# Performance work log

Measured on AMD Instinct MI355X. Metric: run time of the kernel, lower is better.

## Reference

```python
import jax, jax.numpy as jnp
import numpy as np


def setup_inputs() -> dict:
    key = jax.random.key(0)
    k1, k2, k3 = jax.random.split(key, 3)
    B, N, D = 4096, 8192, 1024
    protein_features = jax.random.normal(k1, (B, D), dtype=jnp.float32)
    function_features = jax.random.normal(k2, (N, D), dtype=jnp.float32)
    positive_mask = jax.random.randint(k3, (B, N), 0, 2, dtype=jnp.int32)
    temperature = jnp.zeros((1,), dtype=jnp.float32)  # exp(0) = 1
    return {
        "protein_features": protein_features,
        "function_features": function_features,
        "positive_mask": positive_mask,
        "temperature": temperature,
    }


def reference(protein_features, function_features, positive_mask, temperature):
    # logits: [B, N]
    logits = jnp.matmul(protein_features, function_features.T) / jnp.exp(temperature[0])
    # row-wise logsumexp, computed ONCE per row (the torch loop recomputes it per positive)
    lse = jax.nn.logsumexp(logits, axis=1, keepdims=True)  # [B, 1]
    m = (positive_mask == 1).astype(logits.dtype)          # [B, N]
    n_pos = m.sum()
    # per-pair loss = -pos_logit + logsumexp(row); mean over all positive pairs
    loss_sum = ((lse - logits) * m).sum()
    return jnp.where(n_pos > 0, loss_sum / n_pos, jnp.zeros((), dtype=logits.dtype))
```

## Files before the change

kernel.cpp:

```cpp
#include <hip/hip_runtime.h>
#include <hip/hip_bf16.h>

typedef __attribute__((ext_vector_type(4))) float f32x4;
typedef __attribute__((ext_vector_type(8))) __bf16 bf16x8;
typedef __attribute__((ext_vector_type(8))) unsigned short u16x8;

constexpr int BROWS = 4096;
constexpr int NCOLS = 8192;
constexpr int DK    = 1024;
constexpr int BM = 256, BN = 256, BK = 64;
constexpr int NCB = NCOLS / BN;
constexpr int NKT = DK / BK;
constexpr int NIT = NKT / 2;

__device__ static inline unsigned short f2bf(float f) {
  unsigned int u = __builtin_bit_cast(unsigned int, f);
  u += 0x7FFFu + ((u >> 16) & 1u);
  return (unsigned short)(u >> 16);
}

__device__ static inline void gload16(const void* g, void* l) {
  __builtin_amdgcn_global_load_lds(
      (const __attribute__((address_space(1))) void*)g,
      (__attribute__((address_space(3))) void*)l, 16, 0, 0);
}

__global__ void convert_kernel(const float* __restrict__ src,
                               unsigned short* __restrict__ dst,
                               int n4, int applyScale,
                               const float* __restrict__ temp) {
  float scale = applyScale ? expf(-temp[0]) : 1.0f;
  int i = blockIdx.x * blockDim.x + threadIdx.x;
  if (i >= n4) return;
  float4 v = reinterpret_cast<const float4*>(src)[i];
  ushort4 o;
  o.x = f2bf(v.x * scale);
  o.y = f2bf(v.y * scale);
  o.z = f2bf(v.z * scale);
  o.w = f2bf(v.w * scale);
  reinterpret_cast<ushort4*>(dst)[i] = o;
}

__device__ __forceinline__ void stage_half(const unsigned short* __restrict__ g,
                                           unsigned short* l, int t, int kt) {
#pragma unroll
  for (int p = 0; p < 2; ++p) {
    const int off = p * 8192 + t * 16;
    const int row = off >> 7;
    const int keSw = ((off & 127) >> 1) ^ ((row & 7) << 3);
    gload16(g + (size_t)row * DK + kt * 64 + keSw, l + (off >> 1));
  }
}

#define MFMA_BF16 __builtin_amdgcn_mfma_f32_16x16x32_bf16

#define LDS_FRAG(base, row, kk)                                             \
  __builtin_bit_cast(bf16x8, *reinterpret_cast<const u16x8*>(               \
      &(base)[((row) * 64 + (kk) * 32 + l4 * 8) ^ (((row) & 7) << 3)]))

#define READ_A(b, q)                                              \
  aFr[0][0] = LDS_FRAG(As[b][wm], (2*(q)    )*16 + l15, 0);       \
  aFr[0][1] = LDS_FRAG(As[b][wm], (2*(q)    )*16 + l15, 1);       \
  aFr[1][0] = LDS_FRAG(As[b][wm], (2*(q) + 1)*16 + l15, 0);       \
  aFr[1][1] = LDS_FRAG(As[b][wm], (2*(q) + 1)*16 + l15, 1);

#define READ_B(b)                                                 \
  bFr[0][0] = LDS_FRAG(Bs[b][bhB], brB +  0 + l15, 0);            \
  bFr[0][1] = LDS_FRAG(Bs[b][bhB], brB +  0 + l15, 1);            \
  bFr[1][0] = LDS_FRAG(Bs[b][bhB], brB + 16 + l15, 0);            \
  bFr[1][1] = LDS_FRAG(Bs[b][bhB], brB + 16 + l15, 1);            \
  bFr[2][0] = LDS_FRAG(Bs[b][bhB], brB + 32 + l15, 0);            \
  bFr[2][1] = LDS_FRAG(Bs[b][bhB], brB + 32 + l15, 1);            \
  bFr[3][0] = LDS_FRAG(Bs[b][bhB], brB + 48 + l15, 0);            \
  bFr[3][1] = LDS_FRAG(Bs[b][bhB], brB + 48 + l15, 1);

#define COMPUTE(q)                                                                  \
  __builtin_amdgcn_s_setprio(1);                                                   \
  _Pragma("unroll") for (int mm = 0; mm < 2; ++mm)                                  \
  _Pragma("unroll") for (int n = 0; n < 4; ++n) {                                   \
    acc[2*(q)+mm][n] = MFMA_BF16(aFr[mm][0], bFr[n][0], acc[2*(q)+mm][n], 0, 0, 0); \
    acc[2*(q)+mm][n] = MFMA_BF16(aFr[mm][1], bFr[n][1], acc[2*(q)+mm][n], 0, 0, 0); \
  }                                                                                 \
  __builtin_amdgcn_s_setprio(0);

#define PHASE_BAR                          \
  asm volatile("" ::: "memory");           \
  __builtin_amdgcn_s_barrier();            \
  asm volatile("" ::: "memory");

__global__ __launch_bounds__(512, 2)
void main_kernel(const unsigned short* __restrict__ Pb,
                 const unsigned short* __restrict__ Fb,
                 const int* __restrict__ mask,
                 f32x4* __restrict__ partials) {
  __shared__ __align__(16) unsigned short As[2][2][128 * 64];
  __shared__ __align__(16) unsigned short Bs[2][2][128 * 64];
  __shared__ float redM[4][256], redS[4][256], redP[4][256], redC[4][256];

  const int t    = threadIdx.x;
  const int lane = t & 63;
  const int w    = t >> 6;
  const int wm   = w >> 2;
  const int wn   = w & 3;
  const int l15  = lane & 15;
  const int l4   = lane >> 4;
  const int bhB  = wn >> 1;
  const int brB  = (wn & 1) * 64;

  const int brow = blockIdx.y * BM;
  const int bcol = blockIdx.x * BN;

  const unsigned short* Ag0 = Pb + (size_t)brow * DK;
  const unsigned short* Ag1 = Pb + (size_t)(brow + 128) * DK;
  const unsigned short* Bg0 = Fb + (size_t)bcol * DK;
  const unsigned short* Bg1 = Fb + (size_t)(bcol + 128) * DK;

  f32x4 acc[8][4] = {};
  bf16x8 bFr[4][2];
  bf16x8 aFr[2][2];

  stage_half(Bg0, Bs[0][0], t, 0);
  stage_half(Bg1, Bs[0][1], t, 0);
  stage_half(Ag0, As[0][0], t, 0);
  stage_half(Ag1, As[0][1], t, 0);
  stage_half(Bg0, Bs[1][0], t, 1);
  stage_half(Bg1, Bs[1][1], t, 1);
  asm volatile("s_waitcnt vmcnt(4)" ::: "memory");
  PHASE_BAR;

  for (int i = 0; i < NIT; ++i) {
    const int t1 = 2 * i + 1;
    const bool more = (i < NIT - 1);
    READ_B(0); READ_A(0, 0);
    stage_half(Ag0, As[1][0], t, t1);
    COMPUTE(0); PHASE_BAR;
    READ_A(0, 1);
    stage_half(Ag1, As[1][1], t, t1);
    COMPUTE(1); PHASE_BAR;
    READ_A(0, 2);
    if (more) stage_half(Bg0, Bs[0][0], t, t1 + 1);
    COMPUTE(2); PHASE_BAR;
    READ_A(0, 3);
    if (more) stage_half(Bg1, Bs[0][1], t, t1 + 1);
    COMPUTE(3);
    if (more) { asm volatile("s_waitcnt vmcnt(4)" ::: "memory"); }
    else      { asm volatile("s_waitcnt vmcnt(0)" ::: "memory"); }
    PHASE_BAR;
    READ_B(1); READ_A(1, 0);
    if (more) stage_half(Ag0, As[0][0], t, t1 + 1);
    COMPUTE(0); PHASE_BAR;
    READ_A(1, 1);
    if (more) stage_half(Ag1, As[0][1], t, t1 + 1);
    COMPUTE(1); PHASE_BAR;
    READ_A(1, 2);
    if (more) stage_half(Bg0, Bs[1][0], t, t1 + 2);
    COMPUTE(2); PHASE_BAR;
    READ_A(1, 3);
    if (more) stage_half(Bg1, Bs[1][1], t, t1 + 2);
    COMPUTE(3);
    if (more) { asm volatile("s_waitcnt vmcnt(4)" ::: "memory"); }
    PHASE_BAR;
  }

#pragma unroll
  for (int m = 0; m < 8; ++m) {
#pragma unroll
    for (int r = 0; r < 4; ++r) {
      float v0 = acc[m][0][r], v1 = acc[m][1][r], v2 = acc[m][2][r], v3 = acc[m][3][r];
      float mx = fmaxf(fmaxf(v0, v1), fmaxf(v2, v3));
#pragma unroll
      for (int s = 1; s < 16; s <<= 1) mx = fmaxf(mx, __shfl_xor(mx, s, 64));
      float se = __expf(v0 - mx) + __expf(v1 - mx) + __expf(v2 - mx) + __expf(v3 - mx);

      const int lr = wm * 128 + m * 16 + l4 * 4 + r;
      const int* mrow = mask + (size_t)(brow + lr) * NCOLS + bcol + wn * 64 + l15;
      float ps = 0.f, pc = 0.f;
      if (mrow[0]  == 1) { ps += v0; pc += 1.f; }
      if (mrow[16] == 1) { ps += v1; pc += 1.f; }
      if (mrow[32] == 1) { ps += v2; pc += 1.f; }
      if (mrow[48] == 1) { ps += v3; pc += 1.f; }
#pragma unroll
      for (int s = 1; s < 16; s <<= 1) {
        se += __shfl_xor(se, s, 64);
        ps += __shfl_xor(ps, s, 64);
        pc += __shfl_xor(pc, s, 64);
      }
      if (l15 == 0) {
        redM[wn][lr] = mx;
        redS[wn][lr] = se;
        redP[wn][lr] = ps;
        redC[wn][lr] = pc;
      }
    }
  }
  __syncthreads();

  if (t < 256) {
    float m0 = redM[0][t], m1 = redM[1][t], m2 = redM[2][t], m3 = redM[3][t];
    float m  = fmaxf(fmaxf(m0, m1), fmaxf(m2, m3));
    float s  = redS[0][t] * __expf(m0 - m) + redS[1][t] * __expf(m1 - m)
             + redS[2][t] * __expf(m2 - m) + redS[3][t] * __expf(m3 - m);
    float ps = redP[0][t] + redP[1][t] + redP[2][t] + redP[3][t];
    float pc = redC[0][t] + redC[1][t] + redC[2][t] + redC[3][t];
    f32x4 out4;
    out4.x = m; out4.y = s; out4.z = ps; out4.w = pc;
    partials[(size_t)(brow + t) * NCB + blockIdx.x] = out4;
  }
}

__global__ void row_reduce_kernel(const f32x4* __restrict__ partials,
                                  float* __restrict__ rowContrib,
                                  float* __restrict__ rowCnt) {
  const int row  = blockIdx.x * 4 + (threadIdx.x >> 6);
  const int lane = threadIdx.x & 63;
  f32x4 p = partials[(size_t)row * NCB + (lane & 31)];
  float m = p.x;
#pragma unroll
  for (int s = 1; s < 32; s <<= 1) m = fmaxf(m, __shfl_xor(m, s, 64));
  float se = p.y * __expf(p.x - m);
  float ps = p.z, pc = p.w;
#pragma unroll
  for (int s = 1; s < 32; s <<= 1) {
    se += __shfl_xor(se, s, 64);
    ps += __shfl_xor(ps, s, 64);
    pc += __shfl_xor(pc, s, 64);
  }
  if (lane == 0) {
    float lse = m + logf(se);
    rowContrib[row] = pc * lse - ps;
    rowCnt[row]     = pc;
  }
}

__global__ void final_kernel(const float* __restrict__ rowContrib,
                             const float* __restrict__ rowCnt,
                             float* __restrict__ out) {
  __shared__ double sC[256];
  __shared__ double sN[256];
  double c = 0.0, n = 0.0;
  for (int i = threadIdx.x; i < BROWS; i += 256) {
    c += (double)rowContrib[i];
    n += (double)rowCnt[i];
  }
  sC[threadIdx.x] = c;
  sN[threadIdx.x] = n;
  __syncthreads();
  for (int s = 128; s > 0; s >>= 1) {
    if ((int)threadIdx.x < s) {
      sC[threadIdx.x] += sC[threadIdx.x + s];
      sN[threadIdx.x] += sN[threadIdx.x + s];
    }
    __syncthreads();
  }
  if (threadIdx.x == 0) out[0] = (sN[0] > 0.0) ? (float)(sC[0] / sN[0]) : 0.0f;
}

extern "C" void kernel_launch(void* const* d_in, const int* in_sizes, int n_in,
                              void* d_out, int out_size, void* d_ws, size_t ws_size,
                              hipStream_t stream) {
  const float* P    = (const float*)d_in[0];
  const float* F    = (const float*)d_in[1];
  const int*   mask = (const int*)d_in[2];
  const float* temp = (const float*)d_in[3];
  float* out = (float*)d_out;

  char* ws = (char*)d_ws;
  unsigned short* Pb = (unsigned short*)ws;
  unsigned short* Fb = (unsigned short*)(ws + (size_t)BROWS * DK * 2);
  f32x4* partials    = (f32x4*)(ws + (size_t)(BROWS + NCOLS) * DK * 2);
  float* rowContrib  = (float*)((char*)partials + (size_t)BROWS * NCB * sizeof(f32x4));
  float* rowCnt      = rowContrib + BROWS;

  const int nP4 = BROWS * DK / 4;
  const int nF4 = NCOLS * DK / 4;
  hipLaunchKernelGGL(convert_kernel, dim3(nP4 / 256), dim3(256), 0, stream, P, Pb, nP4, 1, temp);
  hipLaunchKernelGGL(convert_kernel, dim3(nF4 / 256), dim3(256), 0, stream, F, Fb, nF4, 0, temp);
  hipLaunchKernelGGL(main_kernel, dim3(NCOLS / BN, BROWS / BM), dim3(512), 0, stream, Pb, Fb, mask, partials);
  hipLaunchKernelGGL(row_reduce_kernel, dim3(BROWS / 4), dim3(256), 0, stream, partials, rowContrib, rowCnt);
  hipLaunchKernelGGL(final_kernel, dim3(1), dim3(256), 0, stream, rowContrib, rowCnt, out);
}
```

Before: 115.3 us.

## Stage mask tiles into LDS asynchronously and pipeline epilogue processing

The positive-mask tile for each 256x256 block is now loaded with async global-to-LDS copies in 32-row chunks, reusing the A/B operand buffers. The first chunk is issued during the last K iteration and the rest are double-buffered against epilogue processing. Previously the epilogue read the mask with scattered direct global loads after the GEMM. This hides mask-load latency behind compute, at the cost of extra barriers, vmcnt bookkeeping and tighter coupling to the staging schedule.

```diff
diff --git a/kernel.cpp b/kernel.cpp
--- a/kernel.cpp
+++ b/kernel.cpp
@@ -52,6 +52,23 @@
   }
 }
 
+__device__ __forceinline__ void stage_mask(const int* __restrict__ mask,
+                                           unsigned short* as0, unsigned short* bs0,
+                                           int t, int brow, int bcol, int b) {
+#pragma unroll
+  for (int p = 0; p < 8; ++p) {
+    const int off  = p * 8192 + t * 16;
+    const int row  = off >> 10;
+    const int colb = off & 1023;
+    const int grow = brow + ((row < 32) ? (b * 32 + row)
+                                        : (128 + b * 32 + (row - 32)));
+    const int* src = mask + (size_t)grow * NCOLS + bcol + (colb >> 2);
+    char* dst = (row < 32) ? ((char*)as0 + row * 1024 + colb)
+                           : ((char*)bs0 + (row - 32) * 1024 + colb);
+    gload16(src, dst);
+  }
+}
+
 #define MFMA_BF16 __builtin_amdgcn_mfma_f32_16x16x32_bf16
 
 #define LDS_FRAG(base, row, kk)                                             \
@@ -87,6 +104,43 @@
   asm volatile("" ::: "memory");           \
   __builtin_amdgcn_s_barrier();            \
   asm volatile("" ::: "memory");
+
+#define PROCESS(b)                                                            \
+  _Pragma("unroll") for (int mh = 0; mh < 2; ++mh) {                          \
+    const int m = 2 * (b) + mh;                                               \
+    const char* mb = (wm == 0) ? (const char*)As[(b) & 1]                     \
+                               : (const char*)Bs[(b) & 1];                    \
+    _Pragma("unroll") for (int r = 0; r < 4; ++r) {                           \
+      float v0 = acc[m][0][r], v1 = acc[m][1][r],                             \
+            v2 = acc[m][2][r], v3 = acc[m][3][r];                             \
+      float mx = fmaxf(fmaxf(v0, v1), fmaxf(v2, v3));                         \
+      _Pragma("unroll") for (int s = 1; s < 16; s <<= 1)                      \
+        mx = fmaxf(mx, __shfl_xor(mx, s, 64));                                \
+      float se = __expf(v0 - mx) + __expf(v1 - mx)                            \
+               + __expf(v2 - mx) + __expf(v3 - mx);                           \
+      const int lrow = mh * 16 + l4 * 4 + r;                                  \
+      const int cb   = (wn * 64 + l15) * 4;                                   \
+      const int mv0 = *(const int*)(mb + lrow * 1024 + cb);                   \
+      const int mv1 = *(const int*)(mb + lrow * 1024 + cb + 64);              \
+      const int mv2 = *(const int*)(mb + lrow * 1024 + cb + 128);             \
+      const int mv3 = *(const int*)(mb + lrow * 1024 + cb + 192);             \
+      float ps = 0.f, pc = 0.f;                                               \
+      if (mv0 == 1) { ps += v0; pc += 1.f; }                                  \
+      if (mv1 == 1) { ps += v1; pc += 1.f; }                                  \
+      if (mv2 == 1) { ps += v2; pc += 1.f; }                                  \
+      if (mv3 == 1) { ps += v3; pc += 1.f; }                                  \
+      _Pragma("unroll") for (int s = 1; s < 16; s <<= 1) {                    \
+        se += __shfl_xor(se, s, 64);                                          \
+        ps += __shfl_xor(ps, s, 64);                                          \
+        pc += __shfl_xor(pc, s, 64);                                          \
+      }                                                                       \
+      const int lr = wm * 128 + m * 16 + l4 * 4 + r;                          \
+      if (l15 == 0) {                                                         \
+        redM[wn][lr] = mx; redS[wn][lr] = se;                                 \
+        redP[wn][lr] = ps; redC[wn][lr] = pc;                                 \
+      }                                                                       \
+    }                                                                         \
+  }
 
 __global__ __launch_bounds__(512, 2)
 void main_kernel(const unsigned short* __restrict__ Pb,
@@ -148,6 +202,7 @@
     PHASE_BAR;
     READ_B(1); READ_A(1, 0);
     if (more) stage_half(Ag0, As[0][0], t, t1 + 1);
+    else      stage_mask(mask, &As[0][0][0], &Bs[0][0][0], t, brow, bcol, 0);
     COMPUTE(0); PHASE_BAR;
     READ_A(1, 1);
     if (more) stage_half(Ag1, As[0][1], t, t1 + 1);
@@ -162,37 +217,24 @@
     PHASE_BAR;
   }
 
-#pragma unroll
-  for (int m = 0; m < 8; ++m) {
-#pragma unroll
-    for (int r = 0; r < 4; ++r) {
-      float v0 = acc[m][0][r], v1 = acc[m][1][r], v2 = acc[m][2][r], v3 = acc[m][3][r];
-      float mx = fmaxf(fmaxf(v0, v1), fmaxf(v2, v3));
-#pragma unroll
-      for (int s = 1; s < 16; s <<= 1) mx = fmaxf(mx, __shfl_xor(mx, s, 64));
-      float se = __expf(v0 - mx) + __expf(v1 - mx) + __expf(v2 - mx) + __expf(v3 - mx);
-
-      const int lr = wm * 128 + m * 16 + l4 * 4 + r;
-      const int* mrow = mask + (size_t)(brow + lr) * NCOLS + bcol + wn * 64 + l15;
-      float ps = 0.f, pc = 0.f;
-      if (mrow[0]  == 1) { ps += v0; pc += 1.f; }
-      if (mrow[16] == 1) { ps += v1; pc += 1.f; }
-      if (mrow[32] == 1) { ps += v2; pc += 1.f; }
-      if (mrow[48] == 1) { ps += v3; pc += 1.f; }
-#pragma unroll
-      for (int s = 1; s < 16; s <<= 1) {
-        se += __shfl_xor(se, s, 64);
-        ps += __shfl_xor(ps, s, 64);
-        pc += __shfl_xor(pc, s, 64);
-      }
-      if (l15 == 0) {
-        redM[wn][lr] = mx;
-        redS[wn][lr] = se;
-        redP[wn][lr] = ps;
-        redC[wn][lr] = pc;
-      }
-    }
-  }
+  stage_mask(mask, &As[1][0][0], &Bs[1][0][0], t, brow, bcol, 1);
+  asm volatile("s_waitcnt vmcnt(8)" ::: "memory");
+  PHASE_BAR;
+  PROCESS(0)
+  PHASE_BAR;
+  stage_mask(mask, &As[0][0][0], &Bs[0][0][0], t, brow, bcol, 2);
+  asm volatile("s_waitcnt vmcnt(8)" ::: "memory");
+  PHASE_BAR;
+  PROCESS(1)
+  PHASE_BAR;
+  stage_mask(mask, &As[1][0][0], &Bs[1][0][0], t, brow, bcol, 3);
+  asm volatile("s_waitcnt vmcnt(8)" ::: "memory");
+  PHASE_BAR;
+  PROCESS(2)
+  PHASE_BAR;
+  asm volatile("s_waitcnt vmcnt(0)" ::: "memory");
+  PHASE_BAR;
+  PROCESS(3)
   __syncthreads();
 
   if (t < 256) {
```

Measured after the change: 125.1 us. 1.09x slower.

## Prefetch mask tile during GEMM main loop and pack it into LDS bitmasks

Applied to the files above, without the earlier changes.

The mask tile is now loaded with coalesced int4 reads inside the K loop, spread across iterations so the loads overlap with MFMA work. Each row is packed into 256-bit ballot masks stored in LDS. The epilogue reads bits from LDS instead of issuing scattered global int loads after the GEMM. This hides the epilogue's mask-load latency, at the cost of extra VGPRs, extra VMEM traffic in the pipelined loop (which may disturb the vmcnt accounting), and a small LDS allocation.

```diff
diff --git a/kernel.cpp b/kernel.cpp
--- a/kernel.cpp
+++ b/kernel.cpp
@@ -88,6 +88,18 @@
   __builtin_amdgcn_s_barrier();            \
   asm volatile("" ::: "memory");
 
+#define PACKROW(v, row)                                                       \
+  {                                                                           \
+    unsigned long long b0 = __ballot((v).x == 1);                             \
+    unsigned long long b1 = __ballot((v).y == 1);                             \
+    unsigned long long b2 = __ballot((v).z == 1);                             \
+    unsigned long long b3 = __ballot((v).w == 1);                             \
+    if (lane == 0) {                                                          \
+      ulonglong4 o; o.x = b0; o.y = b1; o.z = b2; o.w = b3;                   \
+      *reinterpret_cast<ulonglong4*>(&lbits[(size_t)(row) * 4]) = o;          \
+    }                                                                         \
+  }
+
 __global__ __launch_bounds__(512, 2)
 void main_kernel(const unsigned short* __restrict__ Pb,
                  const unsigned short* __restrict__ Fb,
@@ -95,6 +107,7 @@
                  f32x4* __restrict__ partials) {
   __shared__ __align__(16) unsigned short As[2][2][128 * 64];
   __shared__ __align__(16) unsigned short Bs[2][2][128 * 64];
+  __shared__ __align__(32) unsigned long long lbits[256 * 4];
   __shared__ float redM[4][256], redS[4][256], redP[4][256], redC[4][256];
 
   const int t    = threadIdx.x;
@@ -131,17 +144,24 @@
   for (int i = 0; i < NIT; ++i) {
     const int t1 = 2 * i + 1;
     const bool more = (i < NIT - 1);
+    const int mr = i * 32 + w;
+    int4 va0 = reinterpret_cast<const int4*>(mask + (size_t)(brow + mr) * NCOLS + bcol)[lane];
+    int4 va1 = reinterpret_cast<const int4*>(mask + (size_t)(brow + mr + 8) * NCOLS + bcol)[lane];
     READ_B(0); READ_A(0, 0);
     stage_half(Ag0, As[1][0], t, t1);
     COMPUTE(0); PHASE_BAR;
     READ_A(0, 1);
     stage_half(Ag1, As[1][1], t, t1);
+    PACKROW(va0, mr); PACKROW(va1, mr + 8);
     COMPUTE(1); PHASE_BAR;
+    int4 vb0 = reinterpret_cast<const int4*>(mask + (size_t)(brow + mr + 16) * NCOLS + bcol)[lane];
+    int4 vb1 = reinterpret_cast<const int4*>(mask + (size_t)(brow + mr + 24) * NCOLS + bcol)[lane];
     READ_A(0, 2);
     if (more) stage_half(Bg0, Bs[0][0], t, t1 + 1);
     COMPUTE(2); PHASE_BAR;
     READ_A(0, 3);
     if (more) stage_half(Bg1, Bs[0][1], t, t1 + 1);
+    PACKROW(vb0, mr + 16); PACKROW(vb1, mr + 24);
     COMPUTE(3);
     if (more) { asm volatile("s_waitcnt vmcnt(4)" ::: "memory"); }
     else      { asm volatile("s_waitcnt vmcnt(0)" ::: "memory"); }
@@ -162,6 +182,8 @@
     PHASE_BAR;
   }
 
+  __syncthreads();
+
 #pragma unroll
   for (int m = 0; m < 8; ++m) {
 #pragma unroll
@@ -173,12 +195,13 @@
       float se = __expf(v0 - mx) + __expf(v1 - mx) + __expf(v2 - mx) + __expf(v3 - mx);
 
       const int lr = wm * 128 + m * 16 + l4 * 4 + r;
-      const int* mrow = mask + (size_t)(brow + lr) * NCOLS + bcol + wn * 64 + l15;
+      const unsigned long long wB = lbits[(size_t)lr * 4 + (l15 & 3)];
+      const int bsh = wn * 16 + (l15 >> 2);
       float ps = 0.f, pc = 0.f;
-      if (mrow[0]  == 1) { ps += v0; pc += 1.f; }
-      if (mrow[16] == 1) { ps += v1; pc += 1.f; }
-      if (mrow[32] == 1) { ps += v2; pc += 1.f; }
-      if (mrow[48] == 1) { ps += v3; pc += 1.f; }
+      if ((wB >> (bsh     )) & 1ull) { ps += v0; pc += 1.f; }
+      if ((wB >> (bsh +  4)) & 1ull) { ps += v1; pc += 1.f; }
+      if ((wB >> (bsh +  8)) & 1ull) { ps += v2; pc += 1.f; }
+      if ((wB >> (bsh + 12)) & 1ull) { ps += v3; pc += 1.f; }
 #pragma unroll
       for (int s = 1; s < 16; s <<= 1) {
         se += __shfl_xor(se, s, 64);
```

Measured after the change: 130.1 us. 1.13x slower.
